# Kernel optimization log

Measured on AMD Instinct MI355X. Metric: run time of the kernel, lower is better.

Reference implementation:

```python
import jax, jax.numpy as jnp
import numpy as np

VOCAB, HID, ADIM, B = 20, 128, 3, 32
NP, EP, NM, EM = 50000, 800000, 50000, 800000
IN_DIM = VOCAB + 3  # one-hot residues + 3D pos


def _gcn_conv(x, edge_index, W, b, n):
    # PyG GCNConv: h = XW; add self-loops; sym-normalized scatter-add; + bias
    h = x @ W
    loop = jnp.arange(n, dtype=edge_index.dtype)
    src = jnp.concatenate([edge_index[0], loop])
    dst = jnp.concatenate([edge_index[1], loop])
    deg = jax.ops.segment_sum(jnp.ones_like(dst, dtype=h.dtype), dst, num_segments=n)
    dinv = jnp.where(deg > 0, jax.lax.rsqrt(deg), 0.0)
    norm = dinv[src] * dinv[dst]  # [E+N]
    msg = h[src] * norm[:, None]  # [E+N, HID] dominant memory traffic
    return jax.ops.segment_sum(msg, dst, num_segments=n) + b


def _mean_pool(x, batch, nb):
    s = jax.ops.segment_sum(x, batch, num_segments=nb)
    c = jax.ops.segment_sum(jnp.ones((x.shape[0],), x.dtype), batch, num_segments=nb)
    return s / jnp.maximum(c, 1.0)[:, None]


def setup_inputs() -> dict:
    key = jax.random.key(0)
    ks = jax.random.split(key, 32)
    p = lambda k, shp: jax.random.normal(k, shp, dtype=jnp.float32) * 0.02
    inp = {
        "protein_residue": jax.random.randint(ks[0], (NP,), 0, VOCAB, dtype=jnp.int32),
        "protein_pos": jax.random.normal(ks[1], (NP, 3), dtype=jnp.float32),
        "protein_edge_index": jax.random.randint(ks[2], (2, EP), 0, NP, dtype=jnp.int32),
        "protein_batch": jnp.sort(jax.random.randint(ks[3], (NP,), 0, B, dtype=jnp.int32)),
        "molecule_residue": jax.random.randint(ks[4], (NM,), 0, VOCAB, dtype=jnp.int32),
        "molecule_pos": jax.random.normal(ks[5], (NM, 3), dtype=jnp.float32),
        "molecule_edge_index": jax.random.randint(ks[6], (2, EM), 0, NM, dtype=jnp.int32),
        "molecule_batch": jnp.sort(jax.random.randint(ks[7], (NM,), 0, B, dtype=jnp.int32)),
        "t": jax.random.randint(ks[8], (B,), 0, 1000, dtype=jnp.int32),
        "noisy_action": jax.random.normal(ks[9], (NM, ADIM), dtype=jnp.float32),
        # GCN params
        "Wp1": p(ks[10], (IN_DIM, HID)), "bp1": jnp.zeros((HID,), jnp.float32),
        "Wp2": p(ks[11], (HID, HID)),   "bp2": jnp.zeros((HID,), jnp.float32),
        "Wm1": p(ks[12], (IN_DIM, HID)), "bm1": jnp.zeros((HID,), jnp.float32),
        "Wm2": p(ks[13], (HID, HID)),   "bm2": jnp.zeros((HID,), jnp.float32),
        # timestep MLP
        "Wt1": p(ks[14], (1, HID)),   "bt1": jnp.zeros((HID,), jnp.float32),
        "Wt2": p(ks[15], (HID, HID)), "bt2": jnp.zeros((HID,), jnp.float32),
        # noise predictor: in = 2*HID + ADIM + HID = 387
        "Wn1": p(ks[16], (2 * HID + ADIM + HID, HID)), "bn1": jnp.zeros((HID,), jnp.float32),
        "Wn2": p(ks[17], (HID, ADIM)), "bn2": jnp.zeros((ADIM,), jnp.float32),
    }
    return inp


def reference(protein_residue, protein_pos, protein_edge_index, protein_batch,
              molecule_residue, molecule_pos, molecule_edge_index, molecule_batch,
              t, noisy_action,
              Wp1, bp1, Wp2, bp2, Wm1, bm1, Wm2, bm2,
              Wt1, bt1, Wt2, bt2, Wn1, bn1, Wn2, bn2):
    # protein branch
    x_p = jnp.concatenate([jax.nn.one_hot(protein_residue, VOCAB, dtype=jnp.float32), protein_pos], axis=1)
    x_p = jax.nn.relu(_gcn_conv(x_p, protein_edge_index, Wp1, bp1, NP))
    x_p = jax.nn.relu(_gcn_conv(x_p, protein_edge_index, Wp2, bp2, NP))
    protein_emb = _mean_pool(x_p, protein_batch, B)  # [B, HID]
    # molecule branch
    x_m = jnp.concatenate([jax.nn.one_hot(molecule_residue, VOCAB, dtype=jnp.float32), molecule_pos], axis=1)
    x_m = jax.nn.relu(_gcn_conv(x_m, molecule_edge_index, Wm1, bm1, NM))
    x_m = jax.nn.relu(_gcn_conv(x_m, molecule_edge_index, Wm2, bm2, NM))
    # timestep embedding
    t_emb = jax.nn.relu(t[:, None].astype(jnp.float32) @ Wt1 + bt1) @ Wt2 + bt2  # [B, HID]
    # gather pooled embeddings per molecule node, concat, MLP
    feat = jnp.concatenate([x_m, protein_emb[molecule_batch], t_emb[molecule_batch], noisy_action], axis=1)
    return jax.nn.relu(feat @ Wn1 + bn1) @ Wn2 + bn2  # [NM, ADIM]
```

## Files before the change

kernel.cpp:

```cpp
#include <hip/hip_runtime.h>
#include <hip/hip_bf16.h>

#define HID 128
#define BSH 7
#define CSRCAP 4096
#define PCHUNK 4096
#define HCHUNK 16384

typedef __attribute__((ext_vector_type(8))) short short8v;
typedef __attribute__((ext_vector_type(4))) float f32x4;

#if defined(__has_builtin)
#if __has_builtin(__builtin_amdgcn_cvt_f32_fp8) && __has_builtin(__builtin_amdgcn_cvt_pk_fp8_f32)
#define HAVE_HW_FP8 1
#endif
#endif

__device__ __forceinline__ float4 f4fma(float a, float4 x, float4 y) {
    y.x += a * x.x; y.y += a * x.y; y.z += a * x.z; y.w += a * x.w; return y;
}
__device__ __forceinline__ unsigned f2bf2(float lo, float hi) {
    unsigned ul = __float_as_uint(lo), uh = __float_as_uint(hi);
    ul = (ul + 0x7FFF + ((ul >> 16) & 1)) >> 16;
    uh = (uh + 0x7FFF + ((uh >> 16) & 1)) & 0xFFFF0000u;
    return ul | uh;
}
__device__ __forceinline__ unsigned short f2bf1(float v) {
    unsigned u = __float_as_uint(v);
    u = (u + 0x7FFF + ((u >> 16) & 1)) >> 16;
    return (unsigned short)u;
}
__device__ __forceinline__ float bflo(unsigned u) { return __uint_as_float(u << 16); }
__device__ __forceinline__ float bfhi(unsigned u) { return __uint_as_float(u & 0xFFFF0000u); }
__device__ __forceinline__ float bf2f(unsigned short b) {
    return __uint_as_float(((unsigned)b) << 16);
}
__device__ __forceinline__ short8v zero8() {
    short8v z = {0, 0, 0, 0, 0, 0, 0, 0};
    return z;
}

#ifndef HAVE_HW_FP8
__device__ __forceinline__ unsigned fp8enc_pos(float a) {
    if (a >= 448.f) return 0x7Eu;
    if (a < 0.0009765625f) return 0u;
    unsigned b = __float_as_uint(a);
    int e = (int)(b >> 23) - 127;
    if (e >= -6) {
        unsigned r = b + 0x7FFFFu + ((b >> 20) & 1u);
        e = (int)(r >> 23) - 127;
        unsigned m = (r >> 20) & 7u;
        return ((unsigned)(e + 7) << 3) | m;
    } else {
        int m = (int)(a * 512.f + 0.5f);
        return (unsigned)m;
    }
}
__device__ __forceinline__ float fp8dec1(unsigned u7) {
    float fn = __uint_as_float((u7 + 0x3C0u) << 20);
    float fs = (float)u7 * 0.001953125f;
    return u7 >= 8 ? fn : fs;
}
#endif

__device__ __forceinline__ unsigned enc4(float a, float b, float c, float d) {
#ifdef HAVE_HW_FP8
    int pk = __builtin_amdgcn_cvt_pk_fp8_f32(a, b, 0, false);
    pk = __builtin_amdgcn_cvt_pk_fp8_f32(c, d, pk, true);
    return (unsigned)pk;
#else
    return fp8enc_pos(a) | (fp8enc_pos(b) << 8) | (fp8enc_pos(c) << 16) | (fp8enc_pos(d) << 24);
#endif
}
__device__ __forceinline__ void dec4(unsigned x, float* v) {
#ifdef HAVE_HW_FP8
    v[0] = __builtin_amdgcn_cvt_f32_fp8((int)x, 0);
    v[1] = __builtin_amdgcn_cvt_f32_fp8((int)x, 1);
    v[2] = __builtin_amdgcn_cvt_f32_fp8((int)x, 2);
    v[3] = __builtin_amdgcn_cvt_f32_fp8((int)x, 3);
#else
    v[0] = fp8dec1(x & 0xffu);         v[1] = fp8dec1((x >> 8) & 0xffu);
    v[2] = fp8dec1((x >> 16) & 0xffu); v[3] = fp8dec1(x >> 24);
#endif
}
__device__ __forceinline__ void dec16(uint4 u, float* v) {
    dec4(u.x, v); dec4(u.y, v + 4); dec4(u.z, v + 8); dec4(u.w, v + 12);
}

__global__ __launch_bounds__(256) void k_bhist(const int* __restrict__ d1, int e1,
        const int* __restrict__ d2, int e2, int base2,
        int* __restrict__ bktcnt, long etot) {
    __shared__ int hist[1024];
    int tid = threadIdx.x;
    for (int b = tid; b < 1024; b += 256) hist[b] = 0;
    __syncthreads();
    long start = (long)blockIdx.x * HCHUNK;
    long end = start + HCHUNK; if (end > etot) end = etot;
    for (long i = start + tid; i < end; i += 256) {
        int d = (i < e1) ? d1[i] : d2[i - e1] + base2;
        atomicAdd(&hist[d >> BSH], 1);
    }
    __syncthreads();
    for (int b = tid; b < 1024; b += 256)
        if (hist[b]) atomicAdd(&bktcnt[b], hist[b]);
}

__global__ void k_bscan(const int* __restrict__ bktcnt, int* __restrict__ bofs,
                        int* __restrict__ bcur) {
    __shared__ int s[1024];
    int tid = threadIdx.x;
    int v = bktcnt[tid];
    s[tid] = v; __syncthreads();
    for (int o = 1; o < 1024; o <<= 1) {
        int t = (tid >= o) ? s[tid - o] : 0;
        __syncthreads();
        s[tid] += t;
        __syncthreads();
    }
    int ex = s[tid] - v;
    bofs[tid] = ex;
    bcur[tid] = ex;
    if (tid == 1023) bofs[1024] = s[1023];
}

__global__ __launch_bounds__(256) void k_part(
        const int* __restrict__ s1, const int* __restrict__ d1, int e1,
        const int* __restrict__ s2, const int* __restrict__ d2, int e2, int base2,
        int* __restrict__ bcur, int* __restrict__ pedge, int nb, long etot) {
    __shared__ int hist[1024];
    __shared__ int lofs[1024];
    __shared__ int gb[1024];
    __shared__ int ps[256];
    __shared__ int stage[PCHUNK];
    __shared__ unsigned short sbk[PCHUNK];
    int tid = threadIdx.x;
    long cbase = (long)blockIdx.x * PCHUNK;
    int cnt = (int)((etot - cbase) < PCHUNK ? (etot - cbase) : PCHUNK);
    for (int b = tid; b < 1024; b += 256) hist[b] = 0;
    __syncthreads();
    for (int i = tid; i < cnt; i += 256) {
        long e = cbase + i;
        int d = (e < e1) ? d1[e] : d2[e - e1] + base2;
        atomicAdd(&hist[d >> BSH], 1);
    }
    __syncthreads();
    int h0 = hist[tid * 4], h1 = hist[tid * 4 + 1], h2 = hist[tid * 4 + 2], h3 = hist[tid * 4 + 3];
    int sum = h0 + h1 + h2 + h3;
    ps[tid] = sum; __syncthreads();
    for (int o = 1; o < 256; o <<= 1) {
        int v = (tid >= o) ? ps[tid - o] : 0;
        __syncthreads();
        ps[tid] += v;
        __syncthreads();
    }
    int ex = ps[tid] - sum;
    lofs[tid * 4] = ex; lofs[tid * 4 + 1] = ex + h0;
    lofs[tid * 4 + 2] = ex + h0 + h1; lofs[tid * 4 + 3] = ex + h0 + h1 + h2;
    __syncthreads();
    for (int b = tid; b < nb; b += 256) {
        int c = hist[b];
        gb[b] = c ? atomicAdd(&bcur[b], c) : 0;
    }
    __syncthreads();
    for (int b = tid; b < 1024; b += 256) hist[b] = 0;
    __syncthreads();
    for (int i = tid; i < cnt; i += 256) {
        long e = cbase + i;
        int s, d;
        if (e < e1) { s = s1[e]; d = d1[e]; }
        else { s = s2[e - e1] + base2; d = d2[e - e1] + base2; }
        int b = d >> BSH;
        int p = lofs[b] + atomicAdd(&hist[b], 1);
        stage[p] = (s << BSH) | (d & ((1 << BSH) - 1));
        sbk[p] = (unsigned short)b;
    }
    __syncthreads();
    for (int i = tid; i < cnt; i += 256) {
        int b = sbk[i];
        pedge[gb[b] + (i - lofs[b])] = stage[i];
    }
}

__global__ __launch_bounds__(256) void k_csr(const int* __restrict__ pe,
        const int* __restrict__ bofs, int* __restrict__ csrs,
        int* __restrict__ deg, int* __restrict__ offs, float* __restrict__ dinv,
        const int* __restrict__ res1, const float* __restrict__ pos1,
        const int* __restrict__ res2, const float* __restrict__ pos2,
        int np, int np64, uint4* __restrict__ nrec, int n) {
    __shared__ int lofs2[128];
    __shared__ int lcnt[128];
    __shared__ int lcur[128];
    __shared__ int sc[128];
    __shared__ int ss[CSRCAP];
    int b = blockIdx.x, tid = threadIdx.x;
    int n0 = b << BSH;
    int nn = (n - n0) < 128 ? (n - n0) : 128;
    if (tid < 128) { lcnt[tid] = 0; lcur[tid] = 0; }
    __syncthreads();
    int base = bofs[b], total = bofs[b + 1] - base;
    for (int i = tid; i < total; i += 256)
        atomicAdd(&lcnt[pe[base + i] & ((1 << BSH) - 1)], 1);
    __syncthreads();
    int v = 0;
    if (tid < 128) { v = lcnt[tid]; sc[tid] = v; }
    __syncthreads();
    for (int o = 1; o < 128; o <<= 1) {
        int t = 0;
        if (tid < 128 && tid >= o) t = sc[tid - o];
        __syncthreads();
        if (tid < 128) sc[tid] += t;
        __syncthreads();
    }
    if (tid < 128) lofs2[tid] = sc[tid] - v;
    if (tid < nn) {
        int node = n0 + tid;
        offs[node] = base + sc[tid] - v;
        deg[node] = v;
        float dv = rsqrtf((float)(v + 1));
        dinv[node] = dv;
        const int* res = 0; const float* pos = 0; int bseg = 0; bool valid = false;
        if (node < np) { res = res1; pos = pos1; bseg = 0; valid = true; }
        else if (node >= np64) { res = res2; pos = pos2; bseg = np64; valid = true; }
        if (valid) {
            int lg = node - bseg;
            uint4 rr;
            rr.x = __float_as_uint(dv);
            rr.y = (unsigned)res[lg] | ((unsigned)f2bf1(pos[lg * 3 + 0]) << 16);
            rr.z = (unsigned)f2bf1(pos[lg * 3 + 1]) | ((unsigned)f2bf1(pos[lg * 3 + 2]) << 16);
            rr.w = 0;
            nrec[node] = rr;
        }
    }
    __syncthreads();
    if (total <= CSRCAP) {
        for (int i = tid; i < total; i += 256) {
            int e = pe[base + i];
            int ln = e & ((1 << BSH) - 1);
            int pos_ = lofs2[ln] + atomicAdd(&lcur[ln], 1);
            ss[pos_] = e >> BSH;
        }
        __syncthreads();
        for (int i = tid; i < total; i += 256) csrs[base + i] = ss[i];
    } else {
        for (int i = tid; i < total; i += 256) {
            int e = pe[base + i];
            int ln = e & ((1 << BSH) - 1);
            int pos_ = lofs2[ln] + atomicAdd(&lcur[ln], 1);
            csrs[base + pos_] = e >> BSH;
        }
    }
}

__global__ __launch_bounds__(256) void k_agg23(
        const uint4* __restrict__ nrec, const int* __restrict__ offs,
        const int* __restrict__ deg, const int* __restrict__ csrs,
        int np, int np64, int nm,
        const float* __restrict__ W1a, const float* __restrict__ b1a,
        const float* __restrict__ W1b, const float* __restrict__ b1b,
        unsigned* __restrict__ xout) {
    __shared__ float agg[8][20];
    int grp = threadIdx.x >> 5, lane = threadIdx.x & 31;
    int g = blockIdx.x * 8 + grp;
    const float4 *W4, *bp;
    if (g < np) { W4 = (const float4*)W1a; bp = (const float4*)b1a; }
    else if (g >= np64 && g < np64 + nm) { W4 = (const float4*)W1b; bp = (const float4*)b1b; }
    else return;
    if (lane < 20) agg[grp][lane] = 0.f;
    float sx = 0.f, sy = 0.f, sz = 0.f;
    int s0 = offs[g], m = deg[g];
    for (int i = lane; i < m; i += 32) {
        int s = csrs[s0 + i];
        uint4 r = nrec[s];
        float dv = __uint_as_float(r.x);
        int rs = (int)(r.y & 0xffffu);
        float px = bfhi(r.y);
        float py = bflo(r.z);
        float pz = bfhi(r.z);
        atomicAdd(&agg[grp][rs], dv);
        sx += dv * px; sy += dv * py; sz += dv * pz;
    }
    #pragma unroll
    for (int o = 1; o < 32; o <<= 1) {
        sx += __shfl_xor(sx, o, 32);
        sy += __shfl_xor(sy, o, 32);
        sz += __shfl_xor(sz, o, 32);
    }
    uint4 sr = nrec[g];
    float dd = __uint_as_float(sr.x);
    int rsd = (int)(sr.y & 0xffffu);
    float spx = bfhi(sr.y), spy = bflo(sr.z), spz = bfhi(sr.z);
    float4 w20 = W4[20 * 32 + lane], w21 = W4[21 * 32 + lane], w22 = W4[22 * 32 + lane];
    float4 sm = W4[rsd * 32 + lane];
    sm = f4fma(spx, w20, sm); sm = f4fma(spy, w21, sm); sm = f4fma(spz, w22, sm);
    float4 acc = make_float4(dd * sm.x, dd * sm.y, dd * sm.z, dd * sm.w);
    #pragma unroll
    for (int r = 0; r < 20; ++r)
        acc = f4fma(agg[grp][r], W4[r * 32 + lane], acc);
    acc = f4fma(sx, w20, acc);
    acc = f4fma(sy, w21, acc);
    acc = f4fma(sz, w22, acc);
    float4 b = bp[lane];
    float s16 = 16.f * dd;
    float o0 = s16 * fmaxf(dd * acc.x + b.x, 0.f);
    float o1 = s16 * fmaxf(dd * acc.y + b.y, 0.f);
    float o2 = s16 * fmaxf(dd * acc.z + b.z, 0.f);
    float o3 = s16 * fmaxf(dd * acc.w + b.w, 0.f);
    xout[(size_t)g * 32 + lane] = enc4(o0, o1, o2, o3);
}

__global__ __launch_bounds__(256) void k_agg(
        const uint4* __restrict__ H8, const int* __restrict__ offs,
        const int* __restrict__ deg, const int* __restrict__ csrs,
        const float* __restrict__ dinv,
        int np, int np64, int nm,
        unsigned short* __restrict__ outb) {
    int g = blockIdx.x * 8 + (threadIdx.x >> 5);
    if (g >= np && (g < np64 || g >= np64 + nm)) return;
    int lane = threadIdx.x & 31;
    int q = lane >> 3, l8 = lane & 7;
    float acc[16];
    if (q == 0) {
        uint4 u = H8[(size_t)g * 8 + l8];
        dec16(u, acc);
    } else {
        #pragma unroll
        for (int c = 0; c < 16; ++c) acc[c] = 0.f;
    }
    int s0 = offs[g], m = deg[g];
    for (int c0 = 0; c0 < m; c0 += 32) {
        int rem = m - c0; if (rem > 32) rem = 32;
        int li = lane < rem ? lane : rem - 1;
        int se = csrs[s0 + c0 + li];
        int nquad = (rem + 3) >> 2;
        #pragma unroll 8
        for (int j = 0; j < nquad; ++j) {
            int idx = j * 4 + q;
            bool act = idx < rem;
            int s = __shfl(se, act ? idx : 0, 32);
            uint4 u = H8[(size_t)s * 8 + l8];
            if (act) {
                float v[16]; dec16(u, v);
                #pragma unroll
                for (int c = 0; c < 16; ++c) acc[c] += v[c];
            }
        }
    }
    #pragma unroll
    for (int c = 0; c < 16; ++c) {
        acc[c] += __shfl_xor(acc[c], 8, 32);
        acc[c] += __shfl_xor(acc[c], 16, 32);
    }
    if (q == 0) {
        float di = dinv[g] * 0.0625f;
        uint4 pk0, pk1;
        pk0.x = f2bf2(di * acc[0],  di * acc[1]);
        pk0.y = f2bf2(di * acc[2],  di * acc[3]);
        pk0.z = f2bf2(di * acc[4],  di * acc[5]);
        pk0.w = f2bf2(di * acc[6],  di * acc[7]);
        pk1.x = f2bf2(di * acc[8],  di * acc[9]);
        pk1.y = f2bf2(di * acc[10], di * acc[11]);
        pk1.z = f2bf2(di * acc[12], di * acc[13]);
        pk1.w = f2bf2(di * acc[14], di * acc[15]);
        *(uint4*)&outb[(size_t)g * HID + l8 * 16]     = pk0;
        *(uint4*)&outb[(size_t)g * HID + l8 * 16 + 8] = pk1;
    }
}

__global__ void k_tr(const float* __restrict__ Wa, const float* __restrict__ Wb,
                     const float* __restrict__ Wc,
                     unsigned short* __restrict__ Ta, unsigned short* __restrict__ Tb,
                     unsigned short* __restrict__ Tc) {
    int b = blockIdx.x;
    int col = b & 127, m = b >> 7;
    const float* W = (m == 0) ? Wa : (m == 1 ? Wb : Wc);
    unsigned short* T = (m == 0) ? Ta : (m == 1 ? Tb : Tc);
    int k = threadIdx.x;
    T[col * HID + k] = f2bf1(W[k * HID + col]);
}

__global__ __launch_bounds__(256) void k_gemm(const unsigned short* __restrict__ A,
        const unsigned short* __restrict__ Bt1, const unsigned short* __restrict__ Bt2,
        const float* __restrict__ b2a, const float* __restrict__ b2b,
        int nb1, int np64, int ntot, unsigned short* __restrict__ C) {
    const int tid = threadIdx.x;
    const int wid = tid >> 6;
    const int lane = tid & 63;
    const int l15 = lane & 15, lg = lane >> 4;
    const unsigned short* Bt; const float* bb; int r0;
    if ((int)blockIdx.x < nb1) { Bt = Bt1; bb = b2a; r0 = blockIdx.x * 64; }
    else { Bt = Bt2; bb = b2b; r0 = np64 + ((int)blockIdx.x - nb1) * 64; }
    const int cbase = wid * 32;
    f32x4 acc[4][2] = {};
    #pragma unroll
    for (int ks = 0; ks < 4; ++ks) {
        int kb = ks * 32 + lg * 8;
        short8v b0 = *(const short8v*)&Bt[(size_t)(cbase + l15) * HID + kb];
        short8v b1 = *(const short8v*)&Bt[(size_t)(cbase + 16 + l15) * HID + kb];
        #pragma unroll
        for (int rt = 0; rt < 4; ++rt) {
            int gr = r0 + rt * 16 + l15;
            short8v a = (gr < ntot) ? *(const short8v*)&A[(size_t)gr * HID + kb] : zero8();
            acc[rt][0] = __builtin_amdgcn_mfma_f32_16x16x32_bf16(a, b0, acc[rt][0], 0, 0, 0);
            acc[rt][1] = __builtin_amdgcn_mfma_f32_16x16x32_bf16(a, b1, acc[rt][1], 0, 0, 0);
        }
    }
    float bc0 = bb[cbase + l15], bc1 = bb[cbase + 16 + l15];
    #pragma unroll
    for (int rt = 0; rt < 4; ++rt)
        #pragma unroll
        for (int i = 0; i < 4; ++i) {
            int gr = r0 + rt * 16 + lg * 4 + i;
            if (gr < ntot) {
                C[(size_t)gr * HID + cbase + l15]      = f2bf1(fmaxf(acc[rt][0][i] + bc0, 0.f));
                C[(size_t)gr * HID + cbase + 16 + l15] = f2bf1(fmaxf(acc[rt][1][i] + bc1, 0.f));
            }
        }
}

__global__ void k_pool(const unsigned short* __restrict__ x, const int* __restrict__ batch,
                       float* __restrict__ pool, int* __restrict__ cnt, int n) {
    const int ROWS = 64;
    int start = blockIdx.x * ROWS;
    if (start >= n) return;
    int end = start + ROWS; if (end > n) end = n;
    int c = threadIdx.x;
    float acc = 0.f;
    int cur = batch[start];
    int run = 0;
    for (int r = start; r < end; ++r) {
        int b = batch[r];
        if (b != cur) {
            atomicAdd(&pool[cur * HID + c], acc);
            if (c == 0) atomicAdd(&cnt[cur], run);
            acc = 0.f; run = 0; cur = b;
        }
        acc += bf2f(x[(size_t)r * HID + c]);
        run++;
    }
    atomicAdd(&pool[cur * HID + c], acc);
    if (c == 0) atomicAdd(&cnt[cur], run);
}

__global__ void k_combo2(const int* __restrict__ t, const float* __restrict__ Wt1,
                         const float* __restrict__ bt1, const float* __restrict__ Wt2,
                         const float* __restrict__ bt2,
                         const float* __restrict__ pool, const int* __restrict__ cntb,
                         const float* __restrict__ Wn1, const float* __restrict__ bn1,
                         float* __restrict__ combo) {
    __shared__ float th[HID];
    __shared__ float pe[HID];
    __shared__ float te[HID];
    int b = blockIdx.x, c = threadIdx.x;
    float tv = (float)t[b];
    float hv = tv * Wt1[c] + bt1[c];
    th[c] = hv > 0.f ? hv : 0.f;
    float dcnt = (float)cntb[b]; if (dcnt < 1.f) dcnt = 1.f;
    pe[c] = pool[b * HID + c] / dcnt;
    __syncthreads();
    float s = bt2[c];
    for (int k = 0; k < HID; ++k) s += th[k] * Wt2[k * HID + c];
    te[c] = s;
    __syncthreads();
    const float* Wp = Wn1 + 128 * HID;
    const float* Wt = Wn1 + 256 * HID;
    float o = bn1[c];
    for (int k = 0; k < HID; ++k)
        o += pe[k] * Wp[k * HID + c] + te[k] * Wt[k * HID + c];
    combo[b * HID + c] = o;
}

__global__ __launch_bounds__(256) void k_final(const unsigned short* __restrict__ A,
        const unsigned short* __restrict__ Bt ,
        const float* __restrict__ Wn1, const float* __restrict__ combo,
        const int* __restrict__ mbatch, const float* __restrict__ noisy,
        const float* __restrict__ Wn2, const float* __restrict__ bn2,
        float* __restrict__ out, int n) {
    __shared__ float hsm[64][132];
    const int tid = threadIdx.x;
    const int wid = tid >> 6;
    const int lane = tid & 63;
    const int l15 = lane & 15, lg = lane >> 4;
    const int r0 = blockIdx.x * 64;
    const int cbase = wid * 32;
    f32x4 acc[4][2] = {};
    #pragma unroll
    for (int ks = 0; ks < 4; ++ks) {
        int kb = ks * 32 + lg * 8;
        short8v b0 = *(const short8v*)&Bt[(size_t)(cbase + l15) * HID + kb];
        short8v b1 = *(const short8v*)&Bt[(size_t)(cbase + 16 + l15) * HID + kb];
        #pragma unroll
        for (int rt = 0; rt < 4; ++rt) {
            int gr = r0 + rt * 16 + l15;
            short8v a = (gr < n) ? *(const short8v*)&A[(size_t)gr * HID + kb] : zero8();
            acc[rt][0] = __builtin_amdgcn_mfma_f32_16x16x32_bf16(a, b0, acc[rt][0], 0, 0, 0);
            acc[rt][1] = __builtin_amdgcn_mfma_f32_16x16x32_bf16(a, b1, acc[rt][1], 0, 0, 0);
        }
    }
    const float* Wna = Wn1 + 384 * HID;
    #pragma unroll
    for (int rt = 0; rt < 4; ++rt)
        #pragma unroll
        for (int i = 0; i < 4; ++i) {
            int lr = rt * 16 + lg * 4 + i;
            int gr = r0 + lr;
            if (gr < n) {
                int b = mbatch[gr];
                float na0 = noisy[gr * 3 + 0], na1 = noisy[gr * 3 + 1], na2 = noisy[gr * 3 + 2];
                #pragma unroll
                for (int ct = 0; ct < 2; ++ct) {
                    int col = cbase + ct * 16 + l15;
                    float v = acc[rt][ct][i]
                            + na0 * Wna[col] + na1 * Wna[HID + col] + na2 * Wna[2 * HID + col]
                            + combo[b * HID + col];
                    hsm[lr][col] = v > 0.f ? v : 0.f;
                }
            }
        }
    __syncthreads();
    if (tid < 192) {
        int lr = tid / 3, j = tid - lr * 3;
        int gr = r0 + lr;
        if (gr < n) {
            float s = bn2[j];
            for (int c = 0; c < HID; ++c) s += hsm[lr][c] * Wn2[c * 3 + j];
            out[(size_t)gr * 3 + j] = s;
        }
    }
}

extern "C" void kernel_launch(void* const* d_in, const int* in_sizes, int n_in,
                              void* d_out, int out_size, void* d_ws, size_t ws_size,
                              hipStream_t stream) {
    const int*   p_res  = (const int*)d_in[0];
    const float* p_pos  = (const float*)d_in[1];
    const int*   p_ei   = (const int*)d_in[2];
    const int*   p_bat  = (const int*)d_in[3];
    const int*   m_res  = (const int*)d_in[4];
    const float* m_pos  = (const float*)d_in[5];
    const int*   m_ei   = (const int*)d_in[6];
    const int*   m_bat  = (const int*)d_in[7];
    const int*   t      = (const int*)d_in[8];
    const float* noisy  = (const float*)d_in[9];
    const float* Wp1 = (const float*)d_in[10], *bp1 = (const float*)d_in[11];
    const float* Wp2 = (const float*)d_in[12], *bp2 = (const float*)d_in[13];
    const float* Wm1 = (const float*)d_in[14], *bm1 = (const float*)d_in[15];
    const float* Wm2 = (const float*)d_in[16], *bm2 = (const float*)d_in[17];
    const float* Wt1 = (const float*)d_in[18], *bt1 = (const float*)d_in[19];
    const float* Wt2 = (const float*)d_in[20], *bt2 = (const float*)d_in[21];
    const float* Wn1 = (const float*)d_in[22], *bn1 = (const float*)d_in[23];
    const float* Wn2 = (const float*)d_in[24], *bn2 = (const float*)d_in[25];
    float* out = (float*)d_out;

    const int NP = in_sizes[0];
    const int EP = in_sizes[2] / 2;
    const int NM = in_sizes[4];
    const int EM = in_sizes[6] / 2;
    const int B  = in_sizes[8];
    auto al64 = [](int x) { return (x + 63) & ~63; };

    const int np64 = al64(NP);
    const long ntot_m = (long)np64 + NM;
    const long e2sum = (long)EP + EM;

    auto align256 = [](size_t x) { return (x + 255) & ~(size_t)255; };
    size_t req = 0;
    auto count = [&](size_t nb) { req = align256(req) + nb; };
    count(4ull * ntot_m);
    count(4ull * ntot_m);
    count(4ull * ntot_m);
    count(16ull * ntot_m);
    count(4ull * (1024 + 1025 + 1024));
    count(4ull * e2sum);
    count(4ull * e2sum);
    count(1ull * ntot_m * HID);
    count(2ull * ntot_m * HID);
    count(2ull * ntot_m * HID);
    count(2ull * 3 * HID * HID);
    count(4ull * (size_t)B * (HID + 1));
    count(4ull * (size_t)B * HID);
    bool merged = ws_size >= req + 4096;

    char* ws = (char*)d_ws;
    size_t off = 0;
    auto alloc = [&](size_t nb) { off = align256(off); size_t r = off; off += nb; return r; };

    const int NMAX = NP > NM ? NP : NM;
    const int EMAXs = EP > EM ? EP : EM;
    const long ntot_a = merged ? ntot_m : (long)al64(NMAX);
    const long etot_a = merged ? e2sum : (long)EMAXs;

    int*   deg  = (int*)(ws + alloc(4ull * ntot_a));
    int*   offs = (int*)(ws + alloc(4ull * ntot_a));
    float* dinv = (float*)(ws + alloc(4ull * ntot_a));
    uint4* nrec = (uint4*)(ws + alloc(16ull * ntot_a));
    int*   bktcnt = (int*)(ws + alloc(4ull * (1024 + 1025 + 1024)));
    int*   bofs = bktcnt + 1024;
    int*   bcur = bofs + 1025;
    int*   csre = (int*)(ws + alloc(4ull * etot_a));
    int*   csrs = (int*)(ws + alloc(4ull * etot_a));
    unsigned* hb8 = (unsigned*)(ws + alloc(1ull * ntot_a * HID));
    unsigned short* hb = (unsigned short*)(ws + alloc(2ull * ntot_a * HID));
    unsigned short* hc = (unsigned short*)(ws + alloc(2ull * ntot_a * HID));
    unsigned short* w2ta = (unsigned short*)(ws + alloc(2ull * 3 * HID * HID));
    unsigned short* w2tb = w2ta + HID * HID;
    unsigned short* wn1t = w2ta + 2 * HID * HID;
    float* pool = (float*)(ws + alloc(4ull * (size_t)B * (HID + 1)));
    int*   cntb = (int*)(pool + (size_t)B * HID);
    float* combo = (float*)(ws + alloc(4ull * (size_t)B * HID));

    k_tr<<<384, HID, 0, stream>>>(Wp2, Wm2, Wn1, w2ta, w2tb, wn1t);

    auto run = [&](int np_, int nm_,
                   const int* ei1, int e1, const int* ei2, int e2,
                   const int* res1, const float* pos1, const int* res2, const float* pos2,
                   const float* W1a, const float* b1a, const float* W1b, const float* b1b,
                   const float* b2a, const float* b2b) {
        const int np64_ = al64(np_);
        const int ntot = np64_ + nm_;
        const long etot = (long)e1 + e2;
        const int nb = (ntot + 127) >> BSH;
        const int* s1 = ei1, *d1 = ei1 + e1;
        const int* s2 = ei2, *d2 = ei2 + e2;
        hipMemsetAsync(bktcnt, 0, 4096, stream);
        k_bhist<<<(int)((etot + HCHUNK - 1) / HCHUNK), 256, 0, stream>>>(
            d1, e1, d2, e2, np64_, bktcnt, etot);
        k_bscan<<<1, 1024, 0, stream>>>(bktcnt, bofs, bcur);
        k_part<<<(int)((etot + PCHUNK - 1) / PCHUNK), 256, 0, stream>>>(
            s1, d1, e1, s2, d2, e2, np64_, bcur, csre, nb, etot);
        k_csr<<<nb, 256, 0, stream>>>(csre, bofs, csrs, deg, offs, dinv,
                                      res1, pos1, res2, pos2, np_, np64_, nrec, ntot);
        k_agg23<<<(ntot + 7) / 8, 256, 0, stream>>>(nrec, offs, deg, csrs,
                                                    np_, np64_, nm_,
                                                    W1a, b1a, W1b, b1b, hb8);
        k_agg<<<(ntot + 7) / 8, 256, 0, stream>>>((const uint4*)hb8, offs, deg, csrs, dinv,
                                                  np_, np64_, nm_, hc);
        const int nb1 = np64_ / 64;
        const int nb2 = (nm_ + 63) / 64;
        k_gemm<<<nb1 + nb2, 256, 0, stream>>>(hc, w2ta, w2tb, b2a, b2b, nb1, np64_, ntot, hb);
    };

    if (merged) {
        run(NP, NM, p_ei, EP, m_ei, EM,
            p_res, p_pos, m_res, m_pos,
            Wp1, bp1, Wm1, bm1, bp2, bm2);
        hipMemsetAsync(pool, 0, 4ull * (size_t)B * (HID + 1), stream);
        k_pool<<<(NP + 63) / 64, HID, 0, stream>>>(hb, p_bat, pool, cntb, NP);
        k_combo2<<<B, HID, 0, stream>>>(t, Wt1, bt1, Wt2, bt2, pool, cntb, Wn1, bn1, combo);
        k_final<<<(NM + 63) / 64, 256, 0, stream>>>(hb + (size_t)np64 * HID, wn1t, Wn1, combo,
                                                    m_bat, noisy, Wn2, bn2, out, NM);
    } else {
        run(NP, 0, p_ei, EP, p_ei, 0,
            p_res, p_pos, p_res, p_pos,
            Wp1, bp1, Wp1, bp1, bp2, bp2);
        hipMemsetAsync(pool, 0, 4ull * (size_t)B * (HID + 1), stream);
        k_pool<<<(NP + 63) / 64, HID, 0, stream>>>(hb, p_bat, pool, cntb, NP);
        k_combo2<<<B, HID, 0, stream>>>(t, Wt1, bt1, Wt2, bt2, pool, cntb, Wn1, bn1, combo);
        run(0, NM, m_ei, 0, m_ei, EM,
            m_res, m_pos, m_res, m_pos,
            Wm1, bm1, Wm1, bm1, bm2, bm2);
        k_final<<<(NM + 63) / 64, 256, 0, stream>>>(hb, wn1t, Wn1, combo, m_bat, noisy,
                                                    Wn2, bn2, out, NM);
    }
}
```

Before: 240.7 us.

## Split first GCN layer into 23-dim aggregation plus MFMA bf16 GEMM

```diff
diff --git a/kernel.cpp b/kernel.cpp
--- a/kernel.cpp
+++ b/kernel.cpp
@@ -63,13 +63,11 @@
 }
 #endif
 
-__device__ __forceinline__ unsigned enc4(float a, float b, float c, float d) {
+__device__ __forceinline__ unsigned char enc1(float a) {
 #ifdef HAVE_HW_FP8
-    int pk = __builtin_amdgcn_cvt_pk_fp8_f32(a, b, 0, false);
-    pk = __builtin_amdgcn_cvt_pk_fp8_f32(c, d, pk, true);
-    return (unsigned)pk;
+    return (unsigned char)(__builtin_amdgcn_cvt_pk_fp8_f32(a, 0.f, 0, false) & 0xff);
 #else
-    return fp8enc_pos(a) | (fp8enc_pos(b) << 8) | (fp8enc_pos(c) << 16) | (fp8enc_pos(d) << 24);
+    return (unsigned char)fp8enc_pos(a);
 #endif
 }
 __device__ __forceinline__ void dec4(unsigned x, float* v) {
@@ -251,21 +249,21 @@
     }
 }
 
-__global__ __launch_bounds__(256) void k_agg23(
+__global__ __launch_bounds__(256) void k_agg23c(
         const uint4* __restrict__ nrec, const int* __restrict__ offs,
         const int* __restrict__ deg, const int* __restrict__ csrs,
-        int np, int np64, int nm,
-        const float* __restrict__ W1a, const float* __restrict__ b1a,
-        const float* __restrict__ W1b, const float* __restrict__ b1b,
-        unsigned* __restrict__ xout) {
-    __shared__ float agg[8][20];
+        int np, int np64, int nm, unsigned short* __restrict__ x23) {
+    __shared__ float aggL[8][21];
     int grp = threadIdx.x >> 5, lane = threadIdx.x & 31;
     int g = blockIdx.x * 8 + grp;
-    const float4 *W4, *bp;
-    if (g < np) { W4 = (const float4*)W1a; bp = (const float4*)b1a; }
-    else if (g >= np64 && g < np64 + nm) { W4 = (const float4*)W1b; bp = (const float4*)b1b; }
-    else return;
-    if (lane < 20) agg[grp][lane] = 0.f;
+    int ntot = np64 + nm;
+    if (g >= ntot) return;
+    bool valid = (g < np) || (g >= np64);
+    if (!valid) {
+        if (lane < 16) ((unsigned*)x23)[(size_t)g * 16 + lane] = 0;
+        return;
+    }
+    if (lane < 20) aggL[grp][lane] = 0.f;
     float sx = 0.f, sy = 0.f, sz = 0.f;
     int s0 = offs[g], m = deg[g];
     for (int i = lane; i < m; i += 32) {
@@ -273,39 +271,72 @@
         uint4 r = nrec[s];
         float dv = __uint_as_float(r.x);
         int rs = (int)(r.y & 0xffffu);
-        float px = bfhi(r.y);
-        float py = bflo(r.z);
-        float pz = bfhi(r.z);
-        atomicAdd(&agg[grp][rs], dv);
-        sx += dv * px; sy += dv * py; sz += dv * pz;
-    }
+        atomicAdd(&aggL[grp][rs], dv);
+        sx += dv * bfhi(r.y); sy += dv * bflo(r.z); sz += dv * bfhi(r.z);
+    }
+    uint4 sr = nrec[g];
+    float dd = __uint_as_float(sr.x);
+    if (lane == 0) atomicAdd(&aggL[grp][(int)(sr.y & 0xffffu)], dd);
     #pragma unroll
     for (int o = 1; o < 32; o <<= 1) {
         sx += __shfl_xor(sx, o, 32);
         sy += __shfl_xor(sy, o, 32);
         sz += __shfl_xor(sz, o, 32);
     }
-    uint4 sr = nrec[g];
-    float dd = __uint_as_float(sr.x);
-    int rsd = (int)(sr.y & 0xffffu);
-    float spx = bfhi(sr.y), spy = bflo(sr.z), spz = bfhi(sr.z);
-    float4 w20 = W4[20 * 32 + lane], w21 = W4[21 * 32 + lane], w22 = W4[22 * 32 + lane];
-    float4 sm = W4[rsd * 32 + lane];
-    sm = f4fma(spx, w20, sm); sm = f4fma(spy, w21, sm); sm = f4fma(spz, w22, sm);
-    float4 acc = make_float4(dd * sm.x, dd * sm.y, dd * sm.z, dd * sm.w);
-    #pragma unroll
-    for (int r = 0; r < 20; ++r)
-        acc = f4fma(agg[grp][r], W4[r * 32 + lane], acc);
-    acc = f4fma(sx, w20, acc);
-    acc = f4fma(sy, w21, acc);
-    acc = f4fma(sz, w22, acc);
-    float4 b = bp[lane];
-    float s16 = 16.f * dd;
-    float o0 = s16 * fmaxf(dd * acc.x + b.x, 0.f);
-    float o1 = s16 * fmaxf(dd * acc.y + b.y, 0.f);
-    float o2 = s16 * fmaxf(dd * acc.z + b.z, 0.f);
-    float o3 = s16 * fmaxf(dd * acc.w + b.w, 0.f);
-    xout[(size_t)g * 32 + lane] = enc4(o0, o1, o2, o3);
+    sx += dd * bfhi(sr.y); sy += dd * bflo(sr.z); sz += dd * bfhi(sr.z);
+    float val = 0.f;
+    if (lane < 20) val = aggL[grp][lane];
+    else if (lane == 20) val = sx;
+    else if (lane == 21) val = sy;
+    else if (lane == 22) val = sz;
+    x23[(size_t)g * 32 + lane] = f2bf1(dd * val);
+}
+
+__global__ __launch_bounds__(256) void k_gemm1(const unsigned short* __restrict__ A,
+        const unsigned short* __restrict__ Bt1, const unsigned short* __restrict__ Bt2,
+        const float* __restrict__ b1a, const float* __restrict__ b1b,
+        const float* __restrict__ dinv,
+        int nb1, int np64, int ntot, unsigned* __restrict__ hb8) {
+    __shared__ unsigned char stb[64][144];
+    const int tid = threadIdx.x;
+    const int wid = tid >> 6;
+    const int lane = tid & 63;
+    const int l15 = lane & 15, lg = lane >> 4;
+    const unsigned short* Bt; const float* bb; int r0;
+    if ((int)blockIdx.x < nb1) { Bt = Bt1; bb = b1a; r0 = blockIdx.x * 64; }
+    else { Bt = Bt2; bb = b1b; r0 = np64 + ((int)blockIdx.x - nb1) * 64; }
+    const int cbase = wid * 32;
+    const int kb = lg * 8;
+    f32x4 acc[4][2] = {};
+    short8v b0 = *(const short8v*)&Bt[(size_t)(cbase + l15) * 32 + kb];
+    short8v b1v = *(const short8v*)&Bt[(size_t)(cbase + 16 + l15) * 32 + kb];
+    #pragma unroll
+    for (int rt = 0; rt < 4; ++rt) {
+        int gr = r0 + rt * 16 + l15;
+        short8v a = (gr < ntot) ? *(const short8v*)&A[(size_t)gr * 32 + kb] : zero8();
+        acc[rt][0] = __builtin_amdgcn_mfma_f32_16x16x32_bf16(a, b0, acc[rt][0], 0, 0, 0);
+        acc[rt][1] = __builtin_amdgcn_mfma_f32_16x16x32_bf16(a, b1v, acc[rt][1], 0, 0, 0);
+    }
+    float bc0 = bb[cbase + l15], bc1 = bb[cbase + 16 + l15];
+    #pragma unroll
+    for (int rt = 0; rt < 4; ++rt)
+        #pragma unroll
+        for (int i = 0; i < 4; ++i) {
+            int lr = rt * 16 + lg * 4 + i;
+            int gr = r0 + lr;
+            float dd16 = (gr < ntot) ? 16.f * dinv[gr] : 0.f;
+            stb[lr][cbase + l15]      = enc1(dd16 * fmaxf(acc[rt][0][i] + bc0, 0.f));
+            stb[lr][cbase + 16 + l15] = enc1(dd16 * fmaxf(acc[rt][1][i] + bc1, 0.f));
+        }
+    __syncthreads();
+    #pragma unroll
+    for (int h = 0; h < 2; ++h) {
+        int idx = h * 256 + tid;
+        int r = idx >> 3, q = idx & 7;
+        int gr = r0 + r;
+        if (gr < ntot)
+            *(uint4*)&hb8[(size_t)gr * 32 + q * 4] = *(const uint4*)&stb[r][q * 16];
+    }
 }
 
 __global__ __launch_bounds__(256) void k_agg(
@@ -369,13 +400,23 @@
 __global__ void k_tr(const float* __restrict__ Wa, const float* __restrict__ Wb,
                      const float* __restrict__ Wc,
                      unsigned short* __restrict__ Ta, unsigned short* __restrict__ Tb,
-                     unsigned short* __restrict__ Tc) {
+                     unsigned short* __restrict__ Tc,
+                     const float* __restrict__ W1a, const float* __restrict__ W1b,
+                     unsigned short* __restrict__ T1a, unsigned short* __restrict__ T1b) {
     int b = blockIdx.x;
-    int col = b & 127, m = b >> 7;
-    const float* W = (m == 0) ? Wa : (m == 1 ? Wb : Wc);
-    unsigned short* T = (m == 0) ? Ta : (m == 1 ? Tb : Tc);
     int k = threadIdx.x;
-    T[col * HID + k] = f2bf1(W[k * HID + col]);
+    if (b < 384) {
+        int col = b & 127, m = b >> 7;
+        const float* W = (m == 0) ? Wa : (m == 1 ? Wb : Wc);
+        unsigned short* T = (m == 0) ? Ta : (m == 1 ? Tb : Tc);
+        T[col * HID + k] = f2bf1(W[k * HID + col]);
+    } else {
+        int bb = b - 384;
+        int col = bb & 127, seg = bb >> 7;
+        const float* W = seg ? W1b : W1a;
+        unsigned short* T = seg ? T1b : T1a;
+        if (k < 32) T[col * 32 + k] = (k < 23) ? f2bf1(W[k * HID + col]) : (unsigned short)0;
+    }
 }
 
 __global__ __launch_bounds__(256) void k_gemm(const unsigned short* __restrict__ A,
@@ -575,7 +616,7 @@
     count(1ull * ntot_m * HID);
     count(2ull * ntot_m * HID);
     count(2ull * ntot_m * HID);
-    count(2ull * 3 * HID * HID);
+    count(2ull * (3 * HID * HID + 2 * HID * 32));
     count(4ull * (size_t)B * (HID + 1));
     count(4ull * (size_t)B * HID);
     bool merged = ws_size >= req + 4096;
@@ -601,19 +642,23 @@
     unsigned* hb8 = (unsigned*)(ws + alloc(1ull * ntot_a * HID));
     unsigned short* hb = (unsigned short*)(ws + alloc(2ull * ntot_a * HID));
     unsigned short* hc = (unsigned short*)(ws + alloc(2ull * ntot_a * HID));
-    unsigned short* w2ta = (unsigned short*)(ws + alloc(2ull * 3 * HID * HID));
+    unsigned short* x23 = hc;
+    unsigned short* w2ta = (unsigned short*)(ws + alloc(2ull * (3 * HID * HID + 2 * HID * 32)));
     unsigned short* w2tb = w2ta + HID * HID;
     unsigned short* wn1t = w2ta + 2 * HID * HID;
+    unsigned short* w1ta = w2ta + 3 * HID * HID;
+    unsigned short* w1tb = w1ta + HID * 32;
     float* pool = (float*)(ws + alloc(4ull * (size_t)B * (HID + 1)));
     int*   cntb = (int*)(pool + (size_t)B * HID);
     float* combo = (float*)(ws + alloc(4ull * (size_t)B * HID));
 
-    k_tr<<<384, HID, 0, stream>>>(Wp2, Wm2, Wn1, w2ta, w2tb, wn1t);
+    k_tr<<<640, HID, 0, stream>>>(Wp2, Wm2, Wn1, w2ta, w2tb, wn1t, Wp1, Wm1, w1ta, w1tb);
 
     auto run = [&](int np_, int nm_,
                    const int* ei1, int e1, const int* ei2, int e2,
                    const int* res1, const float* pos1, const int* res2, const float* pos2,
-                   const float* W1a, const float* b1a, const float* W1b, const float* b1b,
+                   const float* b1a, const float* b1b,
+                   const unsigned short* w1A, const unsigned short* w1B,
                    const float* b2a, const float* b2b) {
         const int np64_ = al64(np_);
         const int ntot = np64_ + nm_;
@@ -629,20 +674,21 @@
             s1, d1, e1, s2, d2, e2, np64_, bcur, csre, nb, etot);
         k_csr<<<nb, 256, 0, stream>>>(csre, bofs, csrs, deg, offs, dinv,
                                       res1, pos1, res2, pos2, np_, np64_, nrec, ntot);
-        k_agg23<<<(ntot + 7) / 8, 256, 0, stream>>>(nrec, offs, deg, csrs,
-                                                    np_, np64_, nm_,
-                                                    W1a, b1a, W1b, b1b, hb8);
+        k_agg23c<<<(ntot + 7) / 8, 256, 0, stream>>>(nrec, offs, deg, csrs,
+                                                     np_, np64_, nm_, x23);
+        const int nb1 = np64_ / 64;
+        const int nb2 = (nm_ + 63) / 64;
+        k_gemm1<<<nb1 + nb2, 256, 0, stream>>>(x23, w1A, w1B, b1a, b1b, dinv,
+                                               nb1, np64_, ntot, hb8);
         k_agg<<<(ntot + 7) / 8, 256, 0, stream>>>((const uint4*)hb8, offs, deg, csrs, dinv,
                                                   np_, np64_, nm_, hc);
-        const int nb1 = np64_ / 64;
-        const int nb2 = (nm_ + 63) / 64;
         k_gemm<<<nb1 + nb2, 256, 0, stream>>>(hc, w2ta, w2tb, b2a, b2b, nb1, np64_, ntot, hb);
     };
 
     if (merged) {
         run(NP, NM, p_ei, EP, m_ei, EM,
             p_res, p_pos, m_res, m_pos,
-            Wp1, bp1, Wm1, bm1, bp2, bm2);
+            bp1, bm1, w1ta, w1tb, bp2, bm2);
         hipMemsetAsync(pool, 0, 4ull * (size_t)B * (HID + 1), stream);
         k_pool<<<(NP + 63) / 64, HID, 0, stream>>>(hb, p_bat, pool, cntb, NP);
         k_combo2<<<B, HID, 0, stream>>>(t, Wt1, bt1, Wt2, bt2, pool, cntb, Wn1, bn1, combo);
@@ -651,13 +697,13 @@
     } else {
         run(NP, 0, p_ei, EP, p_ei, 0,
             p_res, p_pos, p_res, p_pos,
-            Wp1, bp1, Wp1, bp1, bp2, bp2);
+            bp1, bp1, w1ta, w1ta, bp2, bp2);
         hipMemsetAsync(pool, 0, 4ull * (size_t)B * (HID + 1), stream);
         k_pool<<<(NP + 63) / 64, HID, 0, stream>>>(hb, p_bat, pool, cntb, NP);
         k_combo2<<<B, HID, 0, stream>>>(t, Wt1, bt1, Wt2, bt2, pool, cntb, Wn1, bn1, combo);
         run(0, NM, m_ei, 0, m_ei, EM,
             m_res, m_pos, m_res, m_pos,
-            Wm1, bm1, Wm1, bm1, bm2, bm2);
+            bm1, bm1, w1tb, w1tb, bm2, bm2);
         k_final<<<(NM + 63) / 64, 256, 0, stream>>>(hb, wn1t, Wn1, combo, m_bat, noisy,
                                                     Wn2, bn2, out, NM);
     }
```

New measurement: 228.8 us. 4.9% less time.
